# Performance work log

Hardware: AMD Instinct MI355X
Metric: run time of the kernel (lower is better)

## Reference

```python
import jax, jax.numpy as jnp
import numpy as np

INTER = 256
TEMPERATURE = 4.0
NEG_FILL = -1e9


def setup_inputs() -> dict:
    key = jax.random.key(0)
    ks = jax.random.split(key, 8)
    B, C, H, W = 8, 512, 64, 64
    x_query = jax.random.normal(ks[0], (B, C, H, W), dtype=jnp.float32)
    x_support = jax.random.normal(ks[1], (B, C, H, W), dtype=jnp.float32)
    support_embedding = jax.random.normal(ks[2], (B, INTER, H, W), dtype=jnp.float32)
    support_mask = jax.random.randint(ks[3], (B, 1, H, W), 0, 2).astype(jnp.float32)
    scale = 1.0 / np.sqrt(C)
    theta_w = jax.random.normal(ks[4], (INTER, C), dtype=jnp.float32) * scale
    theta_b = jax.random.normal(ks[5], (INTER,), dtype=jnp.float32) * 0.01
    phi_w = jax.random.normal(ks[6], (INTER, C), dtype=jnp.float32) * scale
    phi_b = jax.random.normal(ks[7], (INTER,), dtype=jnp.float32) * 0.01
    return {
        "x_query": x_query,
        "x_support": x_support,
        "support_embedding": support_embedding,
        "support_mask": support_mask,
        "theta_w": theta_w,
        "theta_b": theta_b,
        "phi_w": phi_w,
        "phi_b": phi_b,
    }


def reference(x_query, x_support, support_embedding, support_mask, theta_w, theta_b, phi_w, phi_b):
    B, C, H, W = x_query.shape
    N = H * W
    # g_x: [B, N, 256]
    g_x = support_embedding.reshape(B, INTER, N).transpose(0, 2, 1)
    # 1x1 convs == per-pixel linear over channels
    theta_x = jnp.einsum('oc,bcn->bno', theta_w, x_query.reshape(B, C, N)) + theta_b  # [B, N, 256]
    phi_x = jnp.einsum('oc,bcn->bon', phi_w, x_support.reshape(B, C, N)) + phi_b[None, :, None]  # [B, 256, N]
    f = jnp.matmul(theta_x, phi_x)  # [B, N, N]
    mask = support_mask.reshape(B, 1, N)
    f = f * mask
    # equality-based mask fill (matches torch masked_fill(f == 0, -1e9))
    f = jnp.where(f == 0, NEG_FILL, f) / TEMPERATURE
    attn = jax.nn.softmax(f, axis=-1)  # dropout is identity in eval mode
    y = jnp.matmul(attn, g_x)  # [B, N, 256]
    y = y.transpose(0, 2, 1).reshape(B, INTER, H, W)
    return y
```

## Files before the change

kernel.cpp:

```cpp
#include <hip/hip_runtime.h>
#include <hip/hip_fp16.h>
#include <stdint.h>

typedef _Float16 f16x8 __attribute__((ext_vector_type(8)));
typedef _Float16 f16x4 __attribute__((ext_vector_type(4)));
typedef float    f32x4 __attribute__((ext_vector_type(4)));

#define MFMA16(a, b, c) __builtin_amdgcn_mfma_f32_16x16x32_f16(a, b, c, 0, 0, 0)

static constexpr int BN   = 8;
static constexpr int CIN  = 512;
static constexpr int NHW  = 4096;
static constexpr int OD   = 256;
static constexpr int KBLK = 32;

#define RSWZ(row, cb) ((((row) << 7)) + ((cb) ^ (((row) & 7) << 4)))

__device__ __forceinline__ f16x8 cvt8(const float4 a, const float4 b) {
    f16x8 r;
    r[0] = (_Float16)a.x; r[1] = (_Float16)a.y; r[2] = (_Float16)a.z; r[3] = (_Float16)a.w;
    r[4] = (_Float16)b.x; r[5] = (_Float16)b.y; r[6] = (_Float16)b.z; r[7] = (_Float16)b.w;
    return r;
}

__device__ __forceinline__ uint32_t pkh2(float x, float y) {
    union { _Float16 h[2]; uint32_t u; } z;
    z.h[0] = (_Float16)x; z.h[1] = (_Float16)y;
    return z.u;
}

__global__ __launch_bounds__(256)
void wcvt(const float* __restrict__ thw, const float* __restrict__ phw,
          _Float16* __restrict__ wf)
{
    const int i = blockIdx.x * 256 + threadIdx.x;
    const float4 a = ((const float4*)thw)[i];
    const float4 b = ((const float4*)phw)[i];
    f16x4 ra, rb;
    ra[0] = (_Float16)a.x; ra[1] = (_Float16)a.y; ra[2] = (_Float16)a.z; ra[3] = (_Float16)a.w;
    rb[0] = (_Float16)b.x; rb[1] = (_Float16)b.y; rb[2] = (_Float16)b.z; rb[3] = (_Float16)b.w;
    *(f16x4*)(wf + (size_t)i * 4)          = ra;
    *(f16x4*)(wf + 131072 + (size_t)i * 4) = rb;
}

__global__ __launch_bounds__(256)
void prep_gemm(const float* __restrict__ xq, const float* __restrict__ xs,
               const _Float16* __restrict__ wf,
               const float* __restrict__ thb, const float* __restrict__ phb,
               _Float16* __restrict__ Qws, _Float16* __restrict__ Kws)
{
    const int nt = blockIdx.x, z = blockIdx.y;
    const int b = z >> 1, sel = z & 1;
    const float* x        = (sel ? xs : xq) + (size_t)b * CIN * NHW;
    const _Float16* w     = wf + (size_t)sel * (OD * CIN);
    const float* bias     = sel ? phb : thb;
    _Float16* out         = (sel ? Kws : Qws) + (size_t)b * NHW * OD;
    const int n0 = nt * 64;

    __shared__ __align__(16) char Xs[64 * 128];
    __shared__ __align__(16) char Ws[256 * 128];

    const int t    = threadIdx.x;
    const int lane = t & 63, wave = t >> 6;
    const int l16  = lane & 15, lh = lane >> 4;

    f32x4 acc[4][4] = {};

    for (int c0 = 0; c0 < CIN; c0 += 64) {
        #pragma unroll
        for (int rep = 0; rep < 4; ++rep) {
            const int ci = rep * 16 + (t >> 4);
            const int nl = (t & 15) * 4;
            const float4 v = *(const float4*)&x[(size_t)(c0 + ci) * NHW + n0 + nl];
            *(_Float16*)(Xs + RSWZ(nl + 0, ci * 2)) = (_Float16)v.x;
            *(_Float16*)(Xs + RSWZ(nl + 1, ci * 2)) = (_Float16)v.y;
            *(_Float16*)(Xs + RSWZ(nl + 2, ci * 2)) = (_Float16)v.z;
            *(_Float16*)(Xs + RSWZ(nl + 3, ci * 2)) = (_Float16)v.w;
        }
        #pragma unroll
        for (int r = 0; r < 8; ++r) {
            const int u = r * 256 + t;
            const int o = u >> 3, cs8 = (u & 7) * 8;
            const f16x8 v = *(const f16x8*)(w + (size_t)o * CIN + c0 + cs8);
            *(f16x8*)(Ws + RSWZ(o, cs8 * 2)) = v;
        }
        __syncthreads();

        #pragma unroll
        for (int kk = 0; kk < 2; ++kk) {
            f16x8 af[4];
            #pragma unroll
            for (int oo = 0; oo < 4; ++oo)
                af[oo] = *(const f16x8*)(Ws + RSWZ(wave * 64 + oo * 16 + l16, kk * 64 + lh * 16));
            #pragma unroll
            for (int nn = 0; nn < 4; ++nn) {
                const f16x8 bf = *(const f16x8*)(Xs + RSWZ(nn * 16 + l16, kk * 64 + lh * 16));
                #pragma unroll
                for (int oo = 0; oo < 4; ++oo)
                    acc[oo][nn] = MFMA16(af[oo], bf, acc[oo][nn]);
            }
        }
        __syncthreads();
    }

    #pragma unroll
    for (int oo = 0; oo < 4; ++oo) {
        const float4 bi = *(const float4*)&bias[wave * 64 + oo * 16 + lh * 4];
        #pragma unroll
        for (int nn = 0; nn < 4; ++nn) {
            f16x4 v;
            v[0] = (_Float16)(acc[oo][nn][0] + bi.x);
            v[1] = (_Float16)(acc[oo][nn][1] + bi.y);
            v[2] = (_Float16)(acc[oo][nn][2] + bi.z);
            v[3] = (_Float16)(acc[oo][nn][3] + bi.w);
            const int n = n0 + nn * 16 + l16;
            *(f16x4*)&out[(size_t)n * OD + wave * 64 + oo * 16 + lh * 4] = v;
        }
    }
}

__global__ __launch_bounds__(256)
void compact_mask(const float* __restrict__ mask, int* __restrict__ idx,
                  int* __restrict__ nbArr)
{
    const int b = blockIdx.x, t = threadIdx.x;
    const float* mb = mask + (size_t)b * NHW;
    __shared__ int cnt[256];
    __shared__ int pre[257];

    const int base = t * 16;
    float mv[16];
    int c = 0;
    #pragma unroll
    for (int i = 0; i < 16; ++i) { mv[i] = mb[base + i]; c += (mv[i] != 0.0f); }
    cnt[t] = c;
    __syncthreads();
    if (t == 0) {
        int s = 0;
        for (int i = 0; i < 256; ++i) { pre[i] = s; s += cnt[i]; }
        pre[256] = s;
    }
    __syncthreads();
    int o = pre[t];
    #pragma unroll
    for (int i = 0; i < 16; ++i)
        if (mv[i] != 0.0f) idx[(size_t)b * NHW + o++] = base + i;

    const int Nb = pre[256];
    const int Npad = (Nb + 63) & ~63;
    for (int k = Nb + t; k < Npad; k += 256) idx[(size_t)b * NHW + k] = 0;
    if (t == 0) { nbArr[b * 2] = Nb; nbArr[b * 2 + 1] = Npad >> 5; }
}

__global__ __launch_bounds__(256)
void gather_kv(const _Float16* __restrict__ Kws, const float* __restrict__ emb,
               const int* __restrict__ idx, const int* __restrict__ nbArr,
               _Float16* __restrict__ Kc, _Float16* __restrict__ Vc)
{
    const int b = blockIdx.y, k0 = blockIdx.x * 64, t = threadIdx.x;
    const int Nb = nbArr[b * 2];
    const int Npad = (Nb + 63) & ~63;
    if (k0 >= Npad) return;

    __shared__ int sidx[64];
    if (t < 64) sidx[t] = idx[(size_t)b * NHW + k0 + t];
    __syncthreads();

    const _Float16* Kb = Kws + (size_t)b * NHW * OD;
    char* KcB = (char*)(Kc + (size_t)b * NHW * OD);
    #pragma unroll
    for (int r = 0; r < 8; ++r) {
        const int u = r * 256 + t;
        const int row = u >> 5, c16 = u & 31;
        const f16x8 v = *(const f16x8*)(Kb + (size_t)sidx[row] * OD + c16 * 8);
        *(f16x8*)(KcB + (size_t)(k0 + row) * 512 + ((c16 * 16) ^ ((row & 7) << 4))) = v;
    }

    const float* eb = emb + (size_t)b * OD * NHW;
    char* VcB = (char*)(Vc + (size_t)b * OD * NHW);
    #pragma unroll
    for (int r = 0; r < 8; ++r) {
        const int u = r * 256 + t;
        const int o = u >> 3, uc = u & 7;
        const int chunk = uc >> 2, uin = uc & 3;
        float4 a, c;
        #pragma unroll
        for (int i = 0; i < 4; ++i) ((float*)&a)[i] = eb[(size_t)o * NHW + sidx[uc * 8 + i]];
        #pragma unroll
        for (int i = 0; i < 4; ++i) ((float*)&c)[i] = eb[(size_t)o * NHW + sidx[uc * 8 + 4 + i]];
        const f16x8 v = cvt8(a, c);
        *(f16x8*)(VcB + (size_t)o * (NHW * 2) + (size_t)k0 * 2 + chunk * 64
                      + ((uin ^ ((o >> 1) & 3)) * 16)) = v;
    }
}

__device__ __forceinline__ void load_tile(const char* __restrict__ Kb,
                                          const char* __restrict__ Vb,
                                          int j, int t,
                                          f16x8 (&kst)[4], f16x8 (&vst)[4])
{
    const char* kb = Kb + (size_t)j * (KBLK * 512);
    #pragma unroll
    for (int r = 0; r < 4; ++r)
        kst[r] = *(const f16x8*)(kb + (r * 256 + t) * 16);
    #pragma unroll
    for (int r = 0; r < 4; ++r) {
        const int u = r * 256 + t, o = u >> 2, sl = u & 3;
        vst[r] = *(const f16x8*)(Vb + (size_t)o * (NHW * 2) + (size_t)j * 64 + sl * 16);
    }
}

__global__ __launch_bounds__(256, 2)
void flash_attn(const _Float16* __restrict__ Qws, const _Float16* __restrict__ Kc,
                const _Float16* __restrict__ Vc, const int* __restrict__ nbArr,
                float* __restrict__ outp)
{
    const int bid = blockIdx.x;
    const int b = bid & 7, qt = bid >> 3;
    const int t = threadIdx.x, lane = t & 63, wave = t >> 6;
    const int l16 = lane & 15, lh = lane >> 4;

    __shared__ __align__(16) char Kl[2][KBLK * 512];
    __shared__ __align__(16) char Vl[2][OD * 64];

    const _Float16* Qb = Qws + (size_t)b * NHW * OD;
    const char* Kb = (const char*)(Kc + (size_t)b * NHW * OD);
    const char* Vb = (const char*)(Vc + (size_t)b * OD * NHW);
    const int Nb = nbArr[b * 2];
    const int nt = nbArr[b * 2 + 1];

    f16x8 qf[8];
    {
        const _Float16* qrow = Qb + (size_t)(qt * 64 + wave * 16 + l16) * OD + lh * 8;
        #pragma unroll
        for (int kk = 0; kk < 8; ++kk) qf[kk] = *(const f16x8*)(qrow + kk * 32);
    }

    f32x4 accO[16] = {};
    float M = -INFINITY, L = 0.f;

    f16x8 kst[4], vst[4];
    load_tile(Kb, Vb, 0, t, kst, vst);
    #pragma unroll
    for (int r = 0; r < 4; ++r) {
        *(f16x8*)(Kl[0] + (r * 256 + t) * 16) = kst[r];
        *(f16x8*)(Vl[0] + (r * 256 + t) * 16) = vst[r];
    }
    if (nt > 1) load_tile(Kb, Vb, 1, t, kst, vst);
    __syncthreads();

    #pragma unroll 1
    for (int jt = 0; jt < nt; ++jt) {
        const int cur = jt & 1;
        if (jt + 1 < nt) {
            #pragma unroll
            for (int r = 0; r < 4; ++r) {
                *(f16x8*)(Kl[cur ^ 1] + (r * 256 + t) * 16) = kst[r];
                *(f16x8*)(Vl[cur ^ 1] + (r * 256 + t) * 16) = vst[r];
            }
        }
        if (jt + 2 < nt) load_tile(Kb, Vb, jt + 2, t, kst, vst);

        f32x4 S[2] = {};
        #pragma unroll
        for (int ct = 0; ct < 2; ++ct) {
            const int row = ct * 16 + l16;
            #pragma unroll
            for (int kk = 0; kk < 8; ++kk) {
                const f16x8 kf = *(const f16x8*)(Kl[cur] + row * 512
                                     + ((kk * 64 + lh * 16) ^ ((row & 7) << 4)));
                S[ct] = MFMA16(kf, qf[kk], S[ct]);
            }
        }

        float lg[8];
        #pragma unroll
        for (int ct = 0; ct < 2; ++ct)
            #pragma unroll
            for (int r = 0; r < 4; ++r)
                lg[ct * 4 + r] = S[ct][r] * 0.25f;
        if (jt * 32 + 32 > Nb) {
            #pragma unroll
            for (int ct = 0; ct < 2; ++ct)
                #pragma unroll
                for (int r = 0; r < 4; ++r) {
                    const int kg = jt * 32 + ct * 16 + lh * 4 + r;
                    if (kg >= Nb) lg[ct * 4 + r] = -1e30f;
                }
        }

        float m8 = fmaxf(fmaxf(fmaxf(lg[0], lg[1]), fmaxf(lg[2], lg[3])),
                         fmaxf(fmaxf(lg[4], lg[5]), fmaxf(lg[6], lg[7])));
        m8 = fmaxf(m8, __shfl_xor(m8, 16));
        m8 = fmaxf(m8, __shfl_xor(m8, 32));

        if (__any(m8 > M + 8.0f)) {
            const float nm = fmaxf(M, m8);
            const float fac = __expf(M - nm);
            M = nm; L *= fac;
            #pragma unroll
            for (int oo = 0; oo < 16; ++oo)
                #pragma unroll
                for (int r = 0; r < 4; ++r) accO[oo][r] *= fac;
        }

        float p[8];
        float s = 0.f;
        #pragma unroll
        for (int i = 0; i < 8; ++i) { p[i] = __expf(lg[i] - M); s += p[i]; }
        s += __shfl_xor(s, 16);
        s += __shfl_xor(s, 32);
        L += s;

        const uint32_t ps0 = pkh2(p[0], p[1]), ps1 = pkh2(p[2], p[3]);
        const uint32_t ps2 = pkh2(p[4], p[5]), ps3 = pkh2(p[6], p[7]);
        const int src0 = l16 + (((2 * lh) & 3) << 4);
        const int src1 = src0 + 16;
        const uint32_t q0 = __shfl(ps0, src0), q2 = __shfl(ps2, src0);
        const uint32_t q1 = __shfl(ps1, src0), q3 = __shfl(ps3, src0);
        const uint32_t r0 = __shfl(ps0, src1), r2 = __shfl(ps2, src1);
        const uint32_t r1 = __shfl(ps1, src1), r3 = __shfl(ps3, src1);
        const bool hi = (lh & 2) != 0;
        union { uint32_t u[4]; f16x8 v; } pu;
        pu.u[0] = hi ? q2 : q0;
        pu.u[1] = hi ? q3 : q1;
        pu.u[2] = hi ? r2 : r0;
        pu.u[3] = hi ? r3 : r1;
        const f16x8 pf = pu.v;

        #pragma unroll
        for (int oo = 0; oo < 16; ++oo) {
            const int o = oo * 16 + l16;
            const f16x8 vf = *(const f16x8*)(Vl[cur] + o * 64
                                 + ((lh * 16) ^ (((o >> 1) & 3) << 4)));
            accO[oo] = MFMA16(vf, pf, accO[oo]);
        }
        __syncthreads();
    }

    const float rl = 1.0f / fmaxf(L, 1e-30f);
    const int n = qt * 64 + wave * 16 + l16;
    #pragma unroll
    for (int oo = 0; oo < 16; ++oo) {
        #pragma unroll
        for (int r = 0; r < 4; ++r) {
            const int o = oo * 16 + lh * 4 + r;
            outp[((size_t)b * OD + o) * NHW + n] = accO[oo][r] * rl;
        }
    }
}

extern "C" void kernel_launch(void* const* d_in, const int* in_sizes, int n_in,
                              void* d_out, int out_size, void* d_ws, size_t ws_size,
                              hipStream_t stream) {
    const float* xq   = (const float*)d_in[0];
    const float* xs   = (const float*)d_in[1];
    const float* emb  = (const float*)d_in[2];
    const float* mask = (const float*)d_in[3];
    const float* thw  = (const float*)d_in[4];
    const float* thb  = (const float*)d_in[5];
    const float* phw  = (const float*)d_in[6];
    const float* phb  = (const float*)d_in[7];
    float* out = (float*)d_out;

    const size_t szT = (size_t)BN * NHW * OD;
    _Float16* Qws = (_Float16*)d_ws;
    _Float16* Kws = Qws + szT;
    _Float16* Kc  = Kws + szT;
    _Float16* Vc  = Kc + szT;
    _Float16* wf  = Vc + szT;
    int* idxArr   = (int*)(wf + 2 * OD * CIN);
    int* nbArr    = idxArr + (size_t)BN * NHW;

    wcvt<<<dim3(128), 256, 0, stream>>>(thw, phw, wf);
    compact_mask<<<dim3(BN), 256, 0, stream>>>(mask, idxArr, nbArr);
    prep_gemm<<<dim3(64, 16), 256, 0, stream>>>(xq, xs, wf, thb, phb, Qws, Kws);
    gather_kv<<<dim3(64, BN), 256, 0, stream>>>(Kws, emb, idxArr, nbArr, Kc, Vc);
    flash_attn<<<dim3(512), 256, 0, stream>>>(Qws, Kc, Vc, nbArr, out);
}
```

Baseline: 199.4 us.

## Process two query tiles per wave in flash attention to reuse K/V fragments

Each wave now computes 32 query rows (two 16-row MFMA groups) instead of 16, so every K and V fragment loaded from LDS feeds two MFMAs. The grid is halved to 256 blocks, which halves K/V global and LDS traffic per query. In exchange, accumulator register use doubles and launch bounds drop to one block per CU, reducing occupancy and latency hiding.

```diff
diff --git a/kernel.cpp b/kernel.cpp
--- a/kernel.cpp
+++ b/kernel.cpp
@@ -210,7 +210,7 @@
     }
 }
 
-__global__ __launch_bounds__(256, 2)
+__global__ __launch_bounds__(256, 1)
 void flash_attn(const _Float16* __restrict__ Qws, const _Float16* __restrict__ Kc,
                 const _Float16* __restrict__ Vc, const int* __restrict__ nbArr,
                 float* __restrict__ outp)
@@ -229,15 +229,18 @@
     const int Nb = nbArr[b * 2];
     const int nt = nbArr[b * 2 + 1];
 
-    f16x8 qf[8];
-    {
-        const _Float16* qrow = Qb + (size_t)(qt * 64 + wave * 16 + l16) * OD + lh * 8;
-        #pragma unroll
-        for (int kk = 0; kk < 8; ++kk) qf[kk] = *(const f16x8*)(qrow + kk * 32);
-    }
-
-    f32x4 accO[16] = {};
-    float M = -INFINITY, L = 0.f;
+    f16x8 qf[8][2];
+    #pragma unroll
+    for (int g = 0; g < 2; ++g) {
+        const _Float16* qrow = Qb
+            + (size_t)(qt * 128 + wave * 32 + g * 16 + l16) * OD + lh * 8;
+        #pragma unroll
+        for (int kk = 0; kk < 8; ++kk) qf[kk][g] = *(const f16x8*)(qrow + kk * 32);
+    }
+
+    f32x4 accO[16][2] = {};
+    float M0 = -INFINITY, L0 = 0.f;
+    float M1 = -INFINITY, L1 = 0.f;
 
     f16x8 kst[4], vst[4];
     load_tile(Kb, Vb, 0, t, kst, vst);
@@ -261,7 +264,7 @@
         }
         if (jt + 2 < nt) load_tile(Kb, Vb, jt + 2, t, kst, vst);
 
-        f32x4 S[2] = {};
+        f32x4 S[2][2] = {};
         #pragma unroll
         for (int ct = 0; ct < 2; ++ct) {
             const int row = ct * 16 + l16;
@@ -269,83 +272,100 @@
             for (int kk = 0; kk < 8; ++kk) {
                 const f16x8 kf = *(const f16x8*)(Kl[cur] + row * 512
                                      + ((kk * 64 + lh * 16) ^ ((row & 7) << 4)));
-                S[ct] = MFMA16(kf, qf[kk], S[ct]);
+                S[ct][0] = MFMA16(kf, qf[kk][0], S[ct][0]);
+                S[ct][1] = MFMA16(kf, qf[kk][1], S[ct][1]);
             }
         }
 
-        float lg[8];
+        const bool tail = (jt * 32 + 32 > Nb);
+        float lg[8][2];
         #pragma unroll
         for (int ct = 0; ct < 2; ++ct)
             #pragma unroll
-            for (int r = 0; r < 4; ++r)
-                lg[ct * 4 + r] = S[ct][r] * 0.25f;
-        if (jt * 32 + 32 > Nb) {
-            #pragma unroll
-            for (int ct = 0; ct < 2; ++ct)
+            for (int r = 0; r < 4; ++r) {
+                float v0 = S[ct][0][r] * 0.25f;
+                float v1 = S[ct][1][r] * 0.25f;
+                if (tail) {
+                    const int kg = jt * 32 + ct * 16 + lh * 4 + r;
+                    if (kg >= Nb) { v0 = -1e30f; v1 = -1e30f; }
+                }
+                lg[ct * 4 + r][0] = v0;
+                lg[ct * 4 + r][1] = v1;
+            }
+
+        float m80 = lg[0][0], m81 = lg[0][1];
+        #pragma unroll
+        for (int i = 1; i < 8; ++i) { m80 = fmaxf(m80, lg[i][0]); m81 = fmaxf(m81, lg[i][1]); }
+        m80 = fmaxf(m80, __shfl_xor(m80, 16));
+        m80 = fmaxf(m80, __shfl_xor(m80, 32));
+        m81 = fmaxf(m81, __shfl_xor(m81, 16));
+        m81 = fmaxf(m81, __shfl_xor(m81, 32));
+
+        if (__any((m80 > M0 + 8.0f) || (m81 > M1 + 8.0f))) {
+            const float nm0 = fmaxf(M0, m80), nm1 = fmaxf(M1, m81);
+            const float f0 = __expf(M0 - nm0), f1 = __expf(M1 - nm1);
+            M0 = nm0; L0 *= f0; M1 = nm1; L1 *= f1;
+            #pragma unroll
+            for (int oo = 0; oo < 16; ++oo)
                 #pragma unroll
                 for (int r = 0; r < 4; ++r) {
-                    const int kg = jt * 32 + ct * 16 + lh * 4 + r;
-                    if (kg >= Nb) lg[ct * 4 + r] = -1e30f;
+                    accO[oo][0][r] *= f0;
+                    accO[oo][1][r] *= f1;
                 }
         }
 
-        float m8 = fmaxf(fmaxf(fmaxf(lg[0], lg[1]), fmaxf(lg[2], lg[3])),
-                         fmaxf(fmaxf(lg[4], lg[5]), fmaxf(lg[6], lg[7])));
-        m8 = fmaxf(m8, __shfl_xor(m8, 16));
-        m8 = fmaxf(m8, __shfl_xor(m8, 32));
-
-        if (__any(m8 > M + 8.0f)) {
-            const float nm = fmaxf(M, m8);
-            const float fac = __expf(M - nm);
-            M = nm; L *= fac;
-            #pragma unroll
-            for (int oo = 0; oo < 16; ++oo)
-                #pragma unroll
-                for (int r = 0; r < 4; ++r) accO[oo][r] *= fac;
-        }
-
-        float p[8];
-        float s = 0.f;
-        #pragma unroll
-        for (int i = 0; i < 8; ++i) { p[i] = __expf(lg[i] - M); s += p[i]; }
-        s += __shfl_xor(s, 16);
-        s += __shfl_xor(s, 32);
-        L += s;
-
-        const uint32_t ps0 = pkh2(p[0], p[1]), ps1 = pkh2(p[2], p[3]);
-        const uint32_t ps2 = pkh2(p[4], p[5]), ps3 = pkh2(p[6], p[7]);
+        float p0[8], p1[8], s0 = 0.f, s1 = 0.f;
+        #pragma unroll
+        for (int i = 0; i < 8; ++i) {
+            p0[i] = __expf(lg[i][0] - M0); s0 += p0[i];
+            p1[i] = __expf(lg[i][1] - M1); s1 += p1[i];
+        }
+        s0 += __shfl_xor(s0, 16); s0 += __shfl_xor(s0, 32); L0 += s0;
+        s1 += __shfl_xor(s1, 16); s1 += __shfl_xor(s1, 32); L1 += s1;
+
         const int src0 = l16 + (((2 * lh) & 3) << 4);
         const int src1 = src0 + 16;
-        const uint32_t q0 = __shfl(ps0, src0), q2 = __shfl(ps2, src0);
-        const uint32_t q1 = __shfl(ps1, src0), q3 = __shfl(ps3, src0);
-        const uint32_t r0 = __shfl(ps0, src1), r2 = __shfl(ps2, src1);
-        const uint32_t r1 = __shfl(ps1, src1), r3 = __shfl(ps3, src1);
         const bool hi = (lh & 2) != 0;
-        union { uint32_t u[4]; f16x8 v; } pu;
-        pu.u[0] = hi ? q2 : q0;
-        pu.u[1] = hi ? q3 : q1;
-        pu.u[2] = hi ? r2 : r0;
-        pu.u[3] = hi ? r3 : r1;
-        const f16x8 pf = pu.v;
+        f16x8 pf[2];
+        #pragma unroll
+        for (int g = 0; g < 2; ++g) {
+            const float* p = g ? p1 : p0;
+            const uint32_t ps0 = pkh2(p[0], p[1]), ps1 = pkh2(p[2], p[3]);
+            const uint32_t ps2 = pkh2(p[4], p[5]), ps3 = pkh2(p[6], p[7]);
+            const uint32_t a0 = __shfl(ps0, src0), a2 = __shfl(ps2, src0);
+            const uint32_t a1 = __shfl(ps1, src0), a3 = __shfl(ps3, src0);
+            const uint32_t b0 = __shfl(ps0, src1), b2 = __shfl(ps2, src1);
+            const uint32_t b1 = __shfl(ps1, src1), b3 = __shfl(ps3, src1);
+            union { uint32_t u[4]; f16x8 v; } pu;
+            pu.u[0] = hi ? a2 : a0;
+            pu.u[1] = hi ? a3 : a1;
+            pu.u[2] = hi ? b2 : b0;
+            pu.u[3] = hi ? b3 : b1;
+            pf[g] = pu.v;
+        }
 
         #pragma unroll
         for (int oo = 0; oo < 16; ++oo) {
             const int o = oo * 16 + l16;
             const f16x8 vf = *(const f16x8*)(Vl[cur] + o * 64
                                  + ((lh * 16) ^ (((o >> 1) & 3) << 4)));
-            accO[oo] = MFMA16(vf, pf, accO[oo]);
+            accO[oo][0] = MFMA16(vf, pf[0], accO[oo][0]);
+            accO[oo][1] = MFMA16(vf, pf[1], accO[oo][1]);
         }
         __syncthreads();
     }
 
-    const float rl = 1.0f / fmaxf(L, 1e-30f);
-    const int n = qt * 64 + wave * 16 + l16;
+    const float rl0 = 1.0f / fmaxf(L0, 1e-30f);
+    const float rl1 = 1.0f / fmaxf(L1, 1e-30f);
+    const int n0 = qt * 128 + wave * 32 + l16;
     #pragma unroll
     for (int oo = 0; oo < 16; ++oo) {
         #pragma unroll
         for (int r = 0; r < 4; ++r) {
             const int o = oo * 16 + lh * 4 + r;
-            outp[((size_t)b * OD + o) * NHW + n] = accO[oo][r] * rl;
+            float* row = outp + ((size_t)b * OD + o) * NHW;
+            row[n0]      = accO[oo][0][r] * rl0;
+            row[n0 + 16] = accO[oo][1][r] * rl1;
         }
     }
 }
@@ -376,5 +396,5 @@
     compact_mask<<<dim3(BN), 256, 0, stream>>>(mask, idxArr, nbArr);
     prep_gemm<<<dim3(64, 16), 256, 0, stream>>>(xq, xs, wf, thb, phb, Qws, Kws);
     gather_kv<<<dim3(64, BN), 256, 0, stream>>>(Kws, emb, idxArr, nbArr, Kc, Vc);
-    flash_attn<<<dim3(512), 256, 0, stream>>>(Qws, Kc, Vc, nbArr, out);
-}
+    flash_attn<<<dim3(256), 256, 0, stream>>>(Qws, Kc, Vc, nbArr, out);
+}
```

Result: slower. 248.0 us (+24.4%).
